# Optimization experiments

Measured on AMD Instinct MI355X. Metric: run time of the kernel, lower is better.

The kernel has to match this reference:

```python
import jax, jax.numpy as jnp
import numpy as np

# Module hyperparameters (init_kwargs)
NUM_EXPERTS = 8
HIDDEN = 1024
CAP_FACTORS = [0.5, 0.75, 1.0, 1.0, 1.25, 1.25, 1.5, 1.5]


def setup_inputs() -> dict:
    key = jax.random.key(0)
    k1, k2, k3 = jax.random.split(key, 3)
    G, T = 4, 2048
    token_inputs = jax.random.normal(k1, (G, T, HIDDEN), dtype=jnp.float32)
    # RouterWeights = nn.Linear(hidden, num_experts, bias=True)
    W = jax.random.normal(k2, (HIDDEN, NUM_EXPERTS), dtype=jnp.float32) * (1.0 / np.sqrt(HIDDEN))
    b = jax.random.normal(k3, (NUM_EXPERTS,), dtype=jnp.float32) * 0.01
    return {"token_inputs": token_inputs, "W": W, "b": b, "expert_capacity": 256}


def reference(token_inputs, W, b, expert_capacity):
    # token_inputs: [G, T, H]; jitter_noise=0 so no jitter; ignore_padding_tokens=False
    G, T, _ = token_inputs.shape
    logits = jnp.einsum("gth,he->gte", token_inputs, W) + b  # [G, T, E]
    probs = jax.nn.softmax(logits, axis=-1)
    # router z-loss: mean(logsumexp(logits, -1)^2)
    z_loss = jnp.mean(jax.nn.logsumexp(logits, axis=-1) ** 2)

    capacities = [int(expert_capacity * f) for f in CAP_FACTORS]
    max_cap = max(capacities)

    dispatch_slices = []  # each [G, T, max_cap] int32
    combine_slices = []   # each [G, T, max_cap] float32
    for e, cap in enumerate(capacities):
        gate, idx = jax.lax.top_k(probs[:, :, e], cap)  # [G, cap]
        # one_hot(idx, T): [G, cap, T] -> transpose to [G, T, cap]
        oh = jax.nn.one_hot(idx, T, dtype=jnp.int32).transpose(0, 2, 1)  # [G, T, cap]
        oh = jnp.pad(oh, ((0, 0), (0, 0), (0, max_cap - cap)))
        dispatch_slices.append(oh)
        # combine: gate broadcast over tokens dim (as in original code)
        comb = jnp.broadcast_to(gate[:, None, :], (G, T, cap))  # [G, T, cap]
        comb = jnp.pad(comb, ((0, 0), (0, 0), (0, max_cap - cap)))
        combine_slices.append(comb)

    dispatch_mask = jnp.stack(dispatch_slices, axis=1)  # [G, E, T, max_cap]
    combine_array = jnp.stack(combine_slices, axis=1).astype(jnp.float32)  # [G, E, T, max_cap]
    auxiliary_loss = jnp.float32(0.0)
    return dispatch_mask, combine_array, auxiliary_loss, z_loss
```

## Files before the change

kernel.cpp:

```cpp
#include <hip/hip_runtime.h>
#include <hip/hip_bf16.h>
#include <math.h>

#define G 4
#define T 2048
#define H 1024
#define E 8

typedef float f4 __attribute__((ext_vector_type(4)));
typedef int i4v __attribute__((ext_vector_type(4)));

__global__ __launch_bounds__(256) void router_logits(
    const float* __restrict__ x, const float* __restrict__ W,
    const float* __restrict__ b, float* __restrict__ probs,
    float* __restrict__ lse2) {
  int wave = (int)((blockIdx.x * blockDim.x + threadIdx.x) >> 6);
  int lane = threadIdx.x & 63;
  if (wave >= G * T) return;
  const float* xr = x + (size_t)wave * H;

  double acc0 = 0, acc1 = 0, acc2 = 0, acc3 = 0;
  double acc4 = 0, acc5 = 0, acc6 = 0, acc7 = 0;
#pragma unroll
  for (int j = 0; j < 4; ++j) {
    int hbase = j * 256 + lane * 4;
    f4 xv = *(const f4*)(xr + hbase);
#pragma unroll
    for (int k = 0; k < 4; ++k) {
      const float* wr = W + (size_t)(hbase + k) * 8;
      f4 w0 = *(const f4*)(wr);
      f4 w1 = *(const f4*)(wr + 4);
      double xd = (double)xv[k];
      acc0 += xd * (double)w0[0];
      acc1 += xd * (double)w0[1];
      acc2 += xd * (double)w0[2];
      acc3 += xd * (double)w0[3];
      acc4 += xd * (double)w1[0];
      acc5 += xd * (double)w1[1];
      acc6 += xd * (double)w1[2];
      acc7 += xd * (double)w1[3];
    }
  }
#pragma unroll
  for (int off = 32; off >= 1; off >>= 1) {
    acc0 += __shfl_xor(acc0, off);
    acc1 += __shfl_xor(acc1, off);
    acc2 += __shfl_xor(acc2, off);
    acc3 += __shfl_xor(acc3, off);
    acc4 += __shfl_xor(acc4, off);
    acc5 += __shfl_xor(acc5, off);
    acc6 += __shfl_xor(acc6, off);
    acc7 += __shfl_xor(acc7, off);
  }
  if (lane == 0) {
    double l0 = acc0 + (double)b[0], l1 = acc1 + (double)b[1];
    double l2 = acc2 + (double)b[2], l3 = acc3 + (double)b[3];
    double l4 = acc4 + (double)b[4], l5 = acc5 + (double)b[5];
    double l6 = acc6 + (double)b[6], l7 = acc7 + (double)b[7];
    double m = fmax(fmax(fmax(l0, l1), fmax(l2, l3)),
                    fmax(fmax(l4, l5), fmax(l6, l7)));
    double p0 = exp(l0 - m), p1 = exp(l1 - m), p2 = exp(l2 - m),
           p3 = exp(l3 - m), p4 = exp(l4 - m), p5 = exp(l5 - m),
           p6 = exp(l6 - m), p7 = exp(l7 - m);
    double s = ((p0 + p1) + (p2 + p3)) + ((p4 + p5) + (p6 + p7));
    double inv = 1.0 / s;
    f4 v0 = {(float)(p0 * inv), (float)(p1 * inv), (float)(p2 * inv),
             (float)(p3 * inv)};
    f4 v1 = {(float)(p4 * inv), (float)(p5 * inv), (float)(p6 * inv),
             (float)(p7 * inv)};
    *(f4*)(probs + (size_t)wave * 8) = v0;
    *(f4*)(probs + (size_t)wave * 8 + 4) = v1;
    double lse = m + log(s);
    lse2[wave] = (float)(lse * lse);
  }
}

__global__ __launch_bounds__(1024) void topk_sort(
    const float* __restrict__ probs, float* __restrict__ gate,
    int* __restrict__ idx, int max_cap, int ec) {
  __shared__ unsigned long long keys[T];
  int ge = blockIdx.x;
  int g = ge >> 3, e = ge & 7;
  unsigned tid = threadIdx.x;

  for (int t = tid; t < T; t += 1024) {
    float p = probs[((size_t)g * T + t) * 8 + e];
    unsigned int bits = __float_as_uint(p);
    keys[t] = ((unsigned long long)bits << 32) | (unsigned int)(~t);
  }
  __syncthreads();
  for (unsigned k = 2; k <= T; k <<= 1) {
    for (unsigned j = k >> 1; j > 0; j >>= 1) {
      unsigned i = ((tid & ~(j - 1)) << 1) | (tid & (j - 1));
      unsigned ixj = i | j;
      unsigned long long a = keys[i], c = keys[ixj];
      bool desc = ((i & k) == 0);
      if (desc ? (a < c) : (a > c)) {
        keys[i] = c;
        keys[ixj] = a;
      }
      __syncthreads();
    }
  }

  const double factors[8] = {0.5, 0.75, 1.0, 1.0, 1.25, 1.25, 1.5, 1.5};
  int cap = (int)((double)ec * factors[e]);
  for (int c = tid; c < max_cap; c += 1024) {
    size_t o = (size_t)ge * max_cap + c;
    if (c < cap) {
      unsigned long long kk = keys[c];
      gate[o] = __uint_as_float((unsigned)(kk >> 32));
      idx[o] = (int)(~(unsigned)kk);
    } else {
      gate[o] = 0.0f;
      idx[o] = -1;
    }
  }
}

template <int MC4S>
__global__ __launch_bounds__(256) void fill_out(
    const float* __restrict__ gate, const int* __restrict__ idx,
    const float* __restrict__ lse2, float* __restrict__ out, unsigned n4,
    unsigned mc4_rt) {
  const unsigned mc4 = MC4S ? (unsigned)MC4S : mc4_rt;
  unsigned tid = threadIdx.x;

  if (blockIdx.x == 0) {
    __shared__ double red[256];
    double s = 0.0;
    for (int i = tid; i < G * T; i += 256) s += (double)lse2[i];
    red[tid] = s;
    __syncthreads();
    for (int off = 128; off > 0; off >>= 1) {
      if ((int)tid < off) red[tid] += red[tid + off];
      __syncthreads();
    }
    if (tid == 0) {
      size_t base = (size_t)n4 * 8;
      out[base] = 0.0f;
      out[base + 1] = (float)(red[0] / (double)(G * T));
    }
  }

  f4* outD = (f4*)out;
  f4* outC = outD + n4;
  const f4* gate4 = (const f4*)gate;
  const i4v* idx4 = (const i4v*)idx;
  unsigned stride = gridDim.x * 256u;
  for (unsigned i = blockIdx.x * 256u + tid; i < n4; i += stride) {
    unsigned c4 = i % mc4;
    unsigned rem = i / mc4;
    unsigned t = rem & (T - 1);
    unsigned ge = rem >> 11;
    f4 gv = gate4[ge * mc4 + c4];
    i4v iv = idx4[ge * mc4 + c4];
    f4 dv;
    dv.x = (iv.x == (int)t) ? 1.0f : 0.0f;
    dv.y = (iv.y == (int)t) ? 1.0f : 0.0f;
    dv.z = (iv.z == (int)t) ? 1.0f : 0.0f;
    dv.w = (iv.w == (int)t) ? 1.0f : 0.0f;
    outD[i] = dv;
    outC[i] = gv;
  }
}

extern "C" void kernel_launch(void* const* d_in, const int* in_sizes, int n_in,
                              void* d_out, int out_size, void* d_ws,
                              size_t ws_size, hipStream_t stream) {
  const float* x = (const float*)d_in[0];
  const float* W = (const float*)d_in[1];
  const float* b = (const float*)d_in[2];

  long long body = (long long)out_size - 2;
  int max_cap = (int)(body / (2LL * G * E * T));
  if (max_cap <= 0) return;
  int ec = (2 * max_cap) / 3;

  float* ws = (float*)d_ws;
  float* probs = ws;
  float* lse2 = ws + (size_t)G * T * E;
  float* gate = lse2 + (size_t)G * T;
  int* idx = (int*)(gate + (size_t)G * E * max_cap);

  router_logits<<<(G * T) / 4, 256, 0, stream>>>(x, W, b, probs, lse2);
  topk_sort<<<G * E, 1024, 0, stream>>>(probs, gate, idx, max_cap, ec);

  unsigned n4 = (unsigned)((long long)G * E * T * max_cap / 4);
  int blocks = 6144;
  if (max_cap == 384) {
    fill_out<96><<<blocks, 256, 0, stream>>>(gate, idx, lse2, (float*)d_out,
                                             n4, 96u);
  } else {
    fill_out<0><<<blocks, 256, 0, stream>>>(gate, idx, lse2, (float*)d_out, n4,
                                            (unsigned)(max_cap / 4));
  }
}
```

Baseline: 86.55 us.

## Zero dispatch mask alongside sort, then scatter ones instead of compare-filling

```diff
diff --git a/kernel.cpp b/kernel.cpp
--- a/kernel.cpp
+++ b/kernel.cpp
@@ -6,9 +6,9 @@
 #define T 2048
 #define H 1024
 #define E 8
+#define NSORT (G * E)
 
 typedef float f4 __attribute__((ext_vector_type(4)));
-typedef int i4v __attribute__((ext_vector_type(4)));
 
 __global__ __launch_bounds__(256) void router_logits(
     const float* __restrict__ x, const float* __restrict__ W,
@@ -75,58 +75,67 @@
   }
 }
 
-__global__ __launch_bounds__(1024) void topk_sort(
+__global__ __launch_bounds__(1024) void sort_and_zero(
     const float* __restrict__ probs, float* __restrict__ gate,
-    int* __restrict__ idx, int max_cap, int ec) {
+    int* __restrict__ idx, float* __restrict__ out, unsigned n4d, int max_cap,
+    int ec) {
   __shared__ unsigned long long keys[T];
-  int ge = blockIdx.x;
-  int g = ge >> 3, e = ge & 7;
   unsigned tid = threadIdx.x;
-
-  for (int t = tid; t < T; t += 1024) {
-    float p = probs[((size_t)g * T + t) * 8 + e];
-    unsigned int bits = __float_as_uint(p);
-    keys[t] = ((unsigned long long)bits << 32) | (unsigned int)(~t);
-  }
-  __syncthreads();
-  for (unsigned k = 2; k <= T; k <<= 1) {
-    for (unsigned j = k >> 1; j > 0; j >>= 1) {
-      unsigned i = ((tid & ~(j - 1)) << 1) | (tid & (j - 1));
-      unsigned ixj = i | j;
-      unsigned long long a = keys[i], c = keys[ixj];
-      bool desc = ((i & k) == 0);
-      if (desc ? (a < c) : (a > c)) {
-        keys[i] = c;
-        keys[ixj] = a;
+  unsigned bid = blockIdx.x;
+
+  if (bid < NSORT) {
+    int g = bid >> 3, e = bid & 7;
+    for (int t = tid; t < T; t += 1024) {
+      float p = probs[((size_t)g * T + t) * 8 + e];
+      unsigned int bits = __float_as_uint(p);
+      keys[t] = ((unsigned long long)bits << 32) | (unsigned int)(~t);
+    }
+    __syncthreads();
+    for (unsigned k = 2; k <= T; k <<= 1) {
+      for (unsigned j = k >> 1; j > 0; j >>= 1) {
+        unsigned i = ((tid & ~(j - 1)) << 1) | (tid & (j - 1));
+        unsigned ixj = i | j;
+        unsigned long long a = keys[i], c = keys[ixj];
+        bool desc = ((i & k) == 0);
+        if (desc ? (a < c) : (a > c)) {
+          keys[i] = c;
+          keys[ixj] = a;
+        }
+        __syncthreads();
       }
-      __syncthreads();
-    }
-  }
-
-  const double factors[8] = {0.5, 0.75, 1.0, 1.0, 1.25, 1.25, 1.5, 1.5};
-  int cap = (int)((double)ec * factors[e]);
-  for (int c = tid; c < max_cap; c += 1024) {
-    size_t o = (size_t)ge * max_cap + c;
-    if (c < cap) {
-      unsigned long long kk = keys[c];
-      gate[o] = __uint_as_float((unsigned)(kk >> 32));
-      idx[o] = (int)(~(unsigned)kk);
-    } else {
-      gate[o] = 0.0f;
-      idx[o] = -1;
-    }
+    }
+    const double factors[8] = {0.5, 0.75, 1.0, 1.0, 1.25, 1.25, 1.5, 1.5};
+    int cap = (int)((double)ec * factors[e]);
+    for (int c = tid; c < max_cap; c += 1024) {
+      size_t o = (size_t)bid * max_cap + c;
+      if (c < cap) {
+        unsigned long long kk = keys[c];
+        gate[o] = __uint_as_float((unsigned)(kk >> 32));
+        idx[o] = (int)(~(unsigned)kk);
+      } else {
+        gate[o] = 0.0f;
+        idx[o] = -1;
+      }
+    }
+  } else {
+    f4* outD = (f4*)out;
+    f4 z = {0.0f, 0.0f, 0.0f, 0.0f};
+    unsigned stride = (gridDim.x - NSORT) * 1024u;
+    for (unsigned i = (bid - NSORT) * 1024u + tid; i < n4d; i += stride)
+      outD[i] = z;
   }
 }
 
 template <int MC4S>
-__global__ __launch_bounds__(256) void fill_out(
+__global__ __launch_bounds__(256) void scatter_and_combine(
     const float* __restrict__ gate, const int* __restrict__ idx,
-    const float* __restrict__ lse2, float* __restrict__ out, unsigned n4,
-    unsigned mc4_rt) {
+    const float* __restrict__ lse2, float* __restrict__ out, unsigned n4d,
+    unsigned mc4_rt, int max_cap, unsigned scb) {
   const unsigned mc4 = MC4S ? (unsigned)MC4S : mc4_rt;
   unsigned tid = threadIdx.x;
-
-  if (blockIdx.x == 0) {
+  unsigned bid = blockIdx.x;
+
+  if (bid == 0) {
     __shared__ double red[256];
     double s = 0.0;
     for (int i = tid; i < G * T; i += 256) s += (double)lse2[i];
@@ -137,31 +146,34 @@
       __syncthreads();
     }
     if (tid == 0) {
-      size_t base = (size_t)n4 * 8;
-      out[base] = 0.0f;
-      out[base + 1] = (float)(red[0] / (double)(G * T));
-    }
-  }
-
-  f4* outD = (f4*)out;
-  f4* outC = outD + n4;
+      size_t ne = (size_t)n4d * 4;
+      out[2 * ne] = 0.0f;
+      out[2 * ne + 1] = (float)(red[0] / (double)(G * T));
+    }
+    return;
+  }
+  if (bid <= scb) {
+    unsigned s = (bid - 1) * 256u + tid;
+    if (s < (unsigned)(G * E) * (unsigned)max_cap) {
+      unsigned ge = s / (unsigned)max_cap;
+      unsigned c = s - ge * (unsigned)max_cap;
+      int t = idx[s];
+      if (t >= 0)
+        out[((size_t)ge * T + t) * (unsigned)max_cap + c] = 1.0f;
+    }
+    return;
+  }
+
+  f4* outC = (f4*)out + n4d;
   const f4* gate4 = (const f4*)gate;
-  const i4v* idx4 = (const i4v*)idx;
-  unsigned stride = gridDim.x * 256u;
-  for (unsigned i = blockIdx.x * 256u + tid; i < n4; i += stride) {
+  unsigned fb = bid - 1 - scb;
+  unsigned nfb = gridDim.x - 1 - scb;
+  unsigned stride = nfb * 256u;
+  for (unsigned i = fb * 256u + tid; i < n4d; i += stride) {
     unsigned c4 = i % mc4;
     unsigned rem = i / mc4;
-    unsigned t = rem & (T - 1);
     unsigned ge = rem >> 11;
-    f4 gv = gate4[ge * mc4 + c4];
-    i4v iv = idx4[ge * mc4 + c4];
-    f4 dv;
-    dv.x = (iv.x == (int)t) ? 1.0f : 0.0f;
-    dv.y = (iv.y == (int)t) ? 1.0f : 0.0f;
-    dv.z = (iv.z == (int)t) ? 1.0f : 0.0f;
-    dv.w = (iv.w == (int)t) ? 1.0f : 0.0f;
-    outD[i] = dv;
-    outC[i] = gv;
+    outC[i] = gate4[ge * mc4 + c4];
   }
 }
 
@@ -183,16 +195,20 @@
   float* gate = lse2 + (size_t)G * T;
   int* idx = (int*)(gate + (size_t)G * E * max_cap);
 
+  unsigned n4d = (unsigned)((long long)G * E * T * max_cap / 4);
+  unsigned scb = (unsigned)((G * E * max_cap + 255) / 256);
+
   router_logits<<<(G * T) / 4, 256, 0, stream>>>(x, W, b, probs, lse2);
-  topk_sort<<<G * E, 1024, 0, stream>>>(probs, gate, idx, max_cap, ec);
-
-  unsigned n4 = (unsigned)((long long)G * E * T * max_cap / 4);
+  sort_and_zero<<<NSORT + 2048, 1024, 0, stream>>>(probs, gate, idx,
+                                                   (float*)d_out, n4d, max_cap,
+                                                   ec);
   int blocks = 6144;
   if (max_cap == 384) {
-    fill_out<96><<<blocks, 256, 0, stream>>>(gate, idx, lse2, (float*)d_out,
-                                             n4, 96u);
+    scatter_and_combine<96><<<blocks, 256, 0, stream>>>(
+        gate, idx, lse2, (float*)d_out, n4d, 96u, max_cap, scb);
   } else {
-    fill_out<0><<<blocks, 256, 0, stream>>>(gate, idx, lse2, (float*)d_out, n4,
-                                            (unsigned)(max_cap / 4));
-  }
-}
+    scatter_and_combine<0><<<blocks, 256, 0, stream>>>(
+        gate, idx, lse2, (float*)d_out, n4d, (unsigned)(max_cap / 4), max_cap,
+        scb);
+  }
+}
```

Result: faster. 78.65 us (-9.1%).
